# Performance work log

Measured on AMD Instinct MI355X. Metric: run time of the kernel, lower is better.

Reference implementation:

```python
import jax, jax.numpy as jnp
import numpy as np

N, D, O, E = 8192, 1024, 1024, 16

def setup_inputs() -> dict:
    key = jax.random.key(0)
    k1, k2, k3, k4 = jax.random.split(key, 4)
    scale = 1.0 / np.sqrt(D)
    x = jax.random.normal(k1, (N, D), dtype=jnp.float32)
    Wg = jax.random.normal(k2, (E, D), dtype=jnp.float32) * scale
    We = jax.random.normal(k3, (E, O, D), dtype=jnp.float32) * scale
    be = jax.random.normal(k4, (E, O), dtype=jnp.float32) * scale
    return {"x": x, "Wg": Wg, "We": We, "be": be}

def reference(x, Wg, We, be):
    # gate: softmax over experts
    gate_logits = jnp.einsum('nd,ed->ne', x, Wg)          # [N, E]
    gate_weights = jax.nn.softmax(gate_logits, axis=1)    # [N, E]
    # top-1 mask via >= max (ties keep all maxima, matching torch code)
    max_w = jnp.max(gate_weights, axis=1, keepdims=True)
    mask = (gate_weights >= max_w).astype(gate_weights.dtype)
    sw = gate_weights * mask                              # selected weights [N, E]
    # weighted sum of all-expert Linear outputs, fused (no [N,E,O] intermediate)
    out = jnp.einsum('nd,eod,ne->no', x, We, sw) + sw @ be  # [N, O]
    return (out, gate_weights)
```

## Files before the change

kernel.cpp:

```cpp
#include <hip/hip_runtime.h>
#include <hip/hip_bf16.h>

#define NROWS 8192
#define DIM   1024
#define OUTD  1024
#define NE    16
#define BM    128
#define BN    64
#define BK    32
#define MAXT  96
#define NKSTEP (DIM / BK)
#define NTILE  (OUTD / BN)
#define GATEBLKS 512
#define CONVBLKS 2048

typedef short s16x8 __attribute__((ext_vector_type(8)));
typedef float f32x4 __attribute__((ext_vector_type(4)));

__device__ __forceinline__ unsigned f2bf(float f) {
  __hip_bfloat16 h = __float2bfloat16(f);
  return (unsigned)__builtin_bit_cast(unsigned short, h);
}

__device__ __forceinline__ void gload_lds16(const void* g, void* l) {
  __builtin_amdgcn_global_load_lds(
      (const __attribute__((address_space(1))) void*)g,
      (__attribute__((address_space(3))) void*)l, 16, 0, 0);
}

__global__ __launch_bounds__(256) void convert_we_kernel(
    const float* __restrict__ W, ushort* __restrict__ o) {
  size_t base = ((size_t)blockIdx.x * 256 + threadIdx.x) * 8;
  #pragma unroll
  for (int i = 0; i < 4; ++i) {
    size_t idx = base + (size_t)i * ((size_t)CONVBLKS * 256 * 8);
    float4 a = *(const float4*)(W + idx);
    float4 c = *(const float4*)(W + idx + 4);
    unsigned w0 = f2bf(a.x) | (f2bf(a.y) << 16);
    unsigned w1 = f2bf(a.z) | (f2bf(a.w) << 16);
    unsigned w2 = f2bf(c.x) | (f2bf(c.y) << 16);
    unsigned w3 = f2bf(c.z) | (f2bf(c.w) << 16);
    *(uint4*)(o + idx) = make_uint4(w0, w1, w2, w3);
  }
}

__global__ __launch_bounds__(256) void gate_kernel(
    const float* __restrict__ x, const float* __restrict__ Wg,
    float* __restrict__ gate_out, int* __restrict__ eid,
    float* __restrict__ wsel, ushort* __restrict__ xb,
    int* __restrict__ hist_g)
{
  __shared__ __align__(16) float4 wg4[NE * 256];
  __shared__ int hist[NE];
  int t = threadIdx.x;
  int wid = t >> 6, lane = t & 63;
  if (t < NE) hist[t] = 0;
  const float4* wgg = (const float4*)Wg;
  #pragma unroll
  for (int i = 0; i < 16; ++i) wg4[t + i * 256] = wgg[t + i * 256];
  __syncthreads();

  int n0 = blockIdx.x * 16 + wid * 4;

  float acc[4][NE];
  #pragma unroll
  for (int r = 0; r < 4; ++r)
    #pragma unroll
    for (int e = 0; e < NE; ++e) acc[r][e] = 0.f;

  #pragma unroll
  for (int j = 0; j < 4; ++j) {
    float4 xv[4];
    #pragma unroll
    for (int r = 0; r < 4; ++r) {
      xv[r] = *(const float4*)(x + (size_t)(n0 + r) * DIM + j * 256 + 4 * lane);
      unsigned lo = f2bf(xv[r].x) | (f2bf(xv[r].y) << 16);
      unsigned hi = f2bf(xv[r].z) | (f2bf(xv[r].w) << 16);
      *(uint2*)(xb + (size_t)(n0 + r) * DIM + j * 256 + 4 * lane) = make_uint2(lo, hi);
    }
    #pragma unroll
    for (int e = 0; e < NE; ++e) {
      float4 w = wg4[e * 256 + j * 64 + lane];
      #pragma unroll
      for (int r = 0; r < 4; ++r)
        acc[r][e] += xv[r].x * w.x + xv[r].y * w.y + xv[r].z * w.z + xv[r].w * w.w;
    }
  }

  #pragma unroll
  for (int r = 0; r < 4; ++r) {
    int n = n0 + r;
    float v[NE];
    #pragma unroll
    for (int e = 0; e < NE; ++e) v[e] = acc[r][e];
    #pragma unroll
    for (int i = 0; i < 8; ++i) {
      float send = (lane & 32) ? v[i] : v[i + 8];
      float recv = __shfl_xor(send, 32, 64);
      v[i] = ((lane & 32) ? v[i + 8] : v[i]) + recv;
    }
    #pragma unroll
    for (int i = 0; i < 4; ++i) {
      float send = (lane & 16) ? v[i] : v[i + 4];
      float recv = __shfl_xor(send, 16, 64);
      v[i] = ((lane & 16) ? v[i + 4] : v[i]) + recv;
    }
    #pragma unroll
    for (int i = 0; i < 2; ++i) {
      float send = (lane & 8) ? v[i] : v[i + 2];
      float recv = __shfl_xor(send, 8, 64);
      v[i] = ((lane & 8) ? v[i + 2] : v[i]) + recv;
    }
    {
      float send = (lane & 4) ? v[0] : v[1];
      float recv = __shfl_xor(send, 4, 64);
      v[0] = ((lane & 4) ? v[1] : v[0]) + recv;
    }
    v[0] += __shfl_xor(v[0], 2, 64);
    v[0] += __shfl_xor(v[0], 1, 64);
    float lg = v[0];
    int e = ((lane >> 5) & 1) * 8 + ((lane >> 4) & 1) * 4 +
            ((lane >> 3) & 1) * 2 + ((lane >> 2) & 1);
    float m = lg;
    m = fmaxf(m, __shfl_xor(m, 4, 64));
    m = fmaxf(m, __shfl_xor(m, 8, 64));
    m = fmaxf(m, __shfl_xor(m, 16, 64));
    m = fmaxf(m, __shfl_xor(m, 32, 64));
    float p = expf(lg - m);
    float s = p;
    s += __shfl_xor(s, 4, 64);
    s += __shfl_xor(s, 8, 64);
    s += __shfl_xor(s, 16, 64);
    s += __shfl_xor(s, 32, 64);
    float inv = 1.f / s;
    if ((lane & 3) == 0) gate_out[(size_t)n * NE + e] = p * inv;
    unsigned long long msk = __ballot(lg == m);
    if (lane == 0) {
      int fl = __builtin_ctzll(msk);
      int ebest = ((fl >> 5) & 1) * 8 + ((fl >> 4) & 1) * 4 +
                  ((fl >> 3) & 1) * 2 + ((fl >> 2) & 1);
      eid[n] = ebest;
      wsel[n] = inv;
      atomicAdd(&hist[ebest], 1);
    }
  }
  __syncthreads();
  if (t < NE) hist_g[blockIdx.x * NE + t] = hist[t];
}

__global__ __launch_bounds__(256) void plan_kernel(
    const int* __restrict__ hist_g, int* __restrict__ offsets,
    int* __restrict__ cursors, int4* __restrict__ tiles)
{
  __shared__ int part[16][17];
  __shared__ int sh_total;
  int t = threadIdx.x;
  int e = t & 15, chunk = t >> 4;
  int s = 0;
  #pragma unroll
  for (int i = 0; i < 32; ++i) s += hist_g[(chunk * 32 + i) * NE + e];
  part[chunk][e] = s;
  __syncthreads();
  if (t < 64) {
    int lane = t;
    int c = 0;
    if (lane < NE) {
      #pragma unroll
      for (int ch = 0; ch < 16; ++ch) c += part[ch][lane];
    }
    int nt = (c + BM - 1) >> 7;
    int po = c, pt = nt;
    #pragma unroll
    for (int d = 1; d < 16; d <<= 1) {
      int oc = __shfl_up(po, d, 64);
      int ot = __shfl_up(pt, d, 64);
      if (lane >= d) { po += oc; pt += ot; }
    }
    int off = po - c, tbase = pt - nt;
    if (lane < NE) { offsets[lane] = off; cursors[lane] = off; }
    if (lane == NE - 1) { offsets[NE] = po; sh_total = pt; }
    if (lane < NE) {
      int ti = 0;
      for (int m = 0; m < c; m += BM, ++ti)
        tiles[tbase + ti] = make_int4(lane, off + m, (c - m < BM) ? (c - m) : BM, 0);
    }
  }
  __syncthreads();
  for (int i = sh_total + t; i < MAXT; i += 256)
    tiles[i] = make_int4(-1, 0, 0, 0);
}

__global__ __launch_bounds__(256) void scatter_kernel(
    const int* __restrict__ eid, int* __restrict__ cursors,
    int* __restrict__ rowids)
{
  __shared__ int h[NE];
  __shared__ int base[NE];
  int t = threadIdx.x;
  if (t < NE) h[t] = 0;
  __syncthreads();
  int n = blockIdx.x * 256 + t;
  int e = eid[n];
  int local = atomicAdd(&h[e], 1);
  __syncthreads();
  if (t < NE) base[t] = h[t] ? atomicAdd(&cursors[t], h[t]) : 0;
  __syncthreads();
  rowids[base[e] + local] = n;
}

__global__ __launch_bounds__(256, 4) void moe_gemm_kernel(
    const ushort* __restrict__ xb, const ushort* __restrict__ Web,
    const float* __restrict__ be, const int* __restrict__ rowids,
    const float* __restrict__ wsel, const int4* __restrict__ tiles,
    float* __restrict__ out)
{
  __shared__ __align__(16) char lds[3 * 12288];
  __shared__ int   rows_s[BM];
  __shared__ float w_s[BM];

  int4 ti = tiles[blockIdx.x];
  int e = ti.x;
  if (e < 0) return;
  int srow = ti.y, nvalid = ti.z;
  int t = threadIdx.x, lane = t & 63;
  int wid = t >> 6, wm = wid >> 1, wn = wid & 1;
  int ncol0 = blockIdx.y * BN;

  if (t < BM) {
    int valid = t < nvalid;
    int rid = valid ? rowids[srow + t] : 0;
    rows_s[t] = valid ? rid : -1;
    w_s[t] = valid ? wsel[rid] : 0.f;
  }

  int r1 = t >> 2, sl = t & 3;
  int r2 = r1 + 64;
  int cg = sl ^ ((r1 >> 1) & 3);
  int rida1 = (r1 < nvalid) ? rowids[srow + r1] : 0;
  int rida2 = (r2 < nvalid) ? rowids[srow + r2] : 0;
  const ushort* ap1 = xb + (size_t)rida1 * DIM + cg * 8;
  const ushort* ap2 = xb + (size_t)rida2 * DIM + cg * 8;
  const ushort* bp1 = Web + (size_t)e * OUTD * DIM + (size_t)(ncol0 + r1) * DIM + cg * 8;

  f32x4 zero = {0.f, 0.f, 0.f, 0.f};
  f32x4 acc[4][2];
  #pragma unroll
  for (int i = 0; i < 4; ++i)
    #pragma unroll
    for (int j = 0; j < 2; ++j) acc[i][j] = zero;

  auto stage = [&](int bufoff, int koff) {
    char* A = lds + bufoff;
    char* B = A + 8192;
    gload_lds16(ap1 + koff, A + t * 16);
    gload_lds16(ap2 + koff, A + 4096 + t * 16);
    gload_lds16(bp1 + koff, B + t * 16);
  };

  unsigned rl15 = lane & 15, rcg = lane >> 4;
  auto body = [&](int bufoff) {
    const char* A = lds + bufoff;
    const char* B = A + 8192;
    s16x8 af[4], bf_[2];
    #pragma unroll
    for (int f = 0; f < 4; ++f) {
      unsigned rA = wm * 64 + f * 16 + rl15;
      af[f] = *(const s16x8*)(A + rA * 64 + ((rcg ^ ((rA >> 1) & 3)) * 16));
    }
    #pragma unroll
    for (int f = 0; f < 2; ++f) {
      unsigned rB = wn * 32 + f * 16 + rl15;
      bf_[f] = *(const s16x8*)(B + rB * 64 + ((rcg ^ ((rB >> 1) & 3)) * 16));
    }
    #pragma unroll
    for (int fm = 0; fm < 4; ++fm)
      #pragma unroll
      for (int fn = 0; fn < 2; ++fn)
        acc[fm][fn] = __builtin_amdgcn_mfma_f32_16x16x32_bf16(af[fm], bf_[fn], acc[fm][fn], 0, 0, 0);
  };

  asm volatile("s_waitcnt vmcnt(0)" ::: "memory");
  stage(0, 0);
  stage(12288, BK);
  int stg = 24576, cur = 0;

  for (int ks = 0; ks < NKSTEP - 1; ++ks) {
    asm volatile("s_waitcnt vmcnt(3)" ::: "memory");
    __builtin_amdgcn_s_barrier();
    asm volatile("" ::: "memory");
    if (ks < NKSTEP - 2) {
      stage(stg, (ks + 2) * BK);
      stg = (stg == 24576) ? 0 : stg + 12288;
    }
    body(cur);
    cur = (cur == 24576) ? 0 : cur + 12288;
  }
  asm volatile("s_waitcnt vmcnt(0)" ::: "memory");
  __builtin_amdgcn_s_barrier();
  asm volatile("" ::: "memory");
  body(cur);

  int rgrp = lane >> 4;
  #pragma unroll
  for (int fn = 0; fn < 2; ++fn) {
    int col = ncol0 + wn * 32 + fn * 16 + (lane & 15);
    float bev = be[e * OUTD + col];
    #pragma unroll
    for (int fm = 0; fm < 4; ++fm) {
      #pragma unroll
      for (int j = 0; j < 4; ++j) {
        int rl = wm * 64 + fm * 16 + rgrp * 4 + j;
        int orow = rows_s[rl];
        if (orow >= 0) {
          float w = w_s[rl];
          out[(size_t)orow * OUTD + col] = w * (acc[fm][fn][j] + bev);
        }
      }
    }
  }
}

extern "C" void kernel_launch(void* const* d_in, const int* in_sizes, int n_in,
                              void* d_out, int out_size, void* d_ws, size_t ws_size,
                              hipStream_t stream) {
  const float* x  = (const float*)d_in[0];
  const float* Wg = (const float*)d_in[1];
  const float* We = (const float*)d_in[2];
  const float* be = (const float*)d_in[3];
  float* out = (float*)d_out;
  float* gate_out = out + (size_t)NROWS * OUTD;

  char* ws = (char*)d_ws;
  int*  cursors = (int*)ws;
  int*  offsets = (int*)(ws + 64);
  int4* tiles   = (int4*)(ws + 256);
  int*  hist_g  = (int*)(ws + 4096);
  int*  eidp    = (int*)(ws + 40960);
  float* wselp  = (float*)(ws + 40960 + 4 * NROWS);
  int*  rowids  = (int*)(ws + 40960 + 8 * NROWS);
  ushort* xb    = (ushort*)(ws + (1u << 20));
  ushort* Web   = (ushort*)(ws + (1u << 20) + 16777216u);

  hipLaunchKernelGGL(convert_we_kernel, dim3(CONVBLKS), dim3(256), 0, stream, We, Web);
  hipLaunchKernelGGL(gate_kernel, dim3(GATEBLKS), dim3(256), 0, stream,
                     x, Wg, gate_out, eidp, wselp, xb, hist_g);
  hipLaunchKernelGGL(plan_kernel, dim3(1), dim3(256), 0, stream,
                     hist_g, offsets, cursors, tiles);
  hipLaunchKernelGGL(scatter_kernel, dim3(NROWS / 256), dim3(256), 0, stream,
                     eidp, cursors, rowids);
  hipLaunchKernelGGL(moe_gemm_kernel, dim3(MAXT, NTILE), dim3(256), 0, stream,
                     xb, Web, be, rowids, wselp, tiles, out);
}
```

Measured before the change: 231.5 us.

## Widen MoE GEMM tile to 128x128 with 32x32 MFMA and double buffering

The grouped GEMM tile grows from 128x64 to 128x128, and the inner product switches from 16x16x32 to 32x32x16 bf16 MFMA with larger per-wave accumulators. The goal is more arithmetic intensity per LDS load and fewer global reloads of the gathered x rows across column tiles. The triple-buffered, manual-waitcnt pipeline becomes a simpler double buffer with __syncthreads, and the grid is flattened so blocks sharing a row tile run next to each other. The trade-off is higher register pressure, half as many blocks, and less overlap between loads and compute.

```diff
diff --git a/kernel.cpp b/kernel.cpp
--- a/kernel.cpp
+++ b/kernel.cpp
@@ -6,16 +6,16 @@
 #define OUTD  1024
 #define NE    16
 #define BM    128
-#define BN    64
+#define BN    128
 #define BK    32
 #define MAXT  96
 #define NKSTEP (DIM / BK)
-#define NTILE  (OUTD / BN)
+#define NCOL   (OUTD / BN)
 #define GATEBLKS 512
 #define CONVBLKS 2048
 
 typedef short s16x8 __attribute__((ext_vector_type(8)));
-typedef float f32x4 __attribute__((ext_vector_type(4)));
+typedef float f32x16 __attribute__((ext_vector_type(16)));
 
 __device__ __forceinline__ unsigned f2bf(float f) {
   __hip_bfloat16 h = __float2bfloat16(f);
@@ -214,17 +214,18 @@
     const float* __restrict__ wsel, const int4* __restrict__ tiles,
     float* __restrict__ out)
 {
-  __shared__ __align__(16) char lds[3 * 12288];
+  __shared__ __align__(16) char lds[2 * 16384];
   __shared__ int   rows_s[BM];
   __shared__ float w_s[BM];
 
-  int4 ti = tiles[blockIdx.x];
+  int rt = blockIdx.x >> 3, c = blockIdx.x & 7;
+  int4 ti = tiles[rt];
   int e = ti.x;
   if (e < 0) return;
   int srow = ti.y, nvalid = ti.z;
   int t = threadIdx.x, lane = t & 63;
   int wid = t >> 6, wm = wid >> 1, wn = wid & 1;
-  int ncol0 = blockIdx.y * BN;
+  int ncol0 = c * BN;
 
   if (t < BM) {
     int valid = t < nvalid;
@@ -240,14 +241,17 @@
   int rida2 = (r2 < nvalid) ? rowids[srow + r2] : 0;
   const ushort* ap1 = xb + (size_t)rida1 * DIM + cg * 8;
   const ushort* ap2 = xb + (size_t)rida2 * DIM + cg * 8;
-  const ushort* bp1 = Web + (size_t)e * OUTD * DIM + (size_t)(ncol0 + r1) * DIM + cg * 8;
-
-  f32x4 zero = {0.f, 0.f, 0.f, 0.f};
-  f32x4 acc[4][2];
-  #pragma unroll
-  for (int i = 0; i < 4; ++i)
-    #pragma unroll
-    for (int j = 0; j < 2; ++j) acc[i][j] = zero;
+  const ushort* bb  = Web + (size_t)e * OUTD * DIM + (size_t)ncol0 * DIM + cg * 8;
+  const ushort* bp1 = bb + (size_t)r1 * DIM;
+  const ushort* bp2 = bb + (size_t)r2 * DIM;
+
+  f32x16 acc[2][2];
+  #pragma unroll
+  for (int i = 0; i < 2; ++i)
+    #pragma unroll
+    for (int j = 0; j < 2; ++j)
+      #pragma unroll
+      for (int r = 0; r < 16; ++r) acc[i][j][r] = 0.f;
 
   auto stage = [&](int bufoff, int koff) {
     char* A = lds + bufoff;
@@ -255,66 +259,55 @@
     gload_lds16(ap1 + koff, A + t * 16);
     gload_lds16(ap2 + koff, A + 4096 + t * 16);
     gload_lds16(bp1 + koff, B + t * 16);
+    gload_lds16(bp2 + koff, B + 4096 + t * 16);
   };
 
-  unsigned rl15 = lane & 15, rcg = lane >> 4;
+  unsigned l31 = lane & 31, lhi = lane >> 5;
   auto body = [&](int bufoff) {
     const char* A = lds + bufoff;
     const char* B = A + 8192;
-    s16x8 af[4], bf_[2];
-    #pragma unroll
-    for (int f = 0; f < 4; ++f) {
-      unsigned rA = wm * 64 + f * 16 + rl15;
-      af[f] = *(const s16x8*)(A + rA * 64 + ((rcg ^ ((rA >> 1) & 3)) * 16));
-    }
-    #pragma unroll
-    for (int f = 0; f < 2; ++f) {
-      unsigned rB = wn * 32 + f * 16 + rl15;
-      bf_[f] = *(const s16x8*)(B + rB * 64 + ((rcg ^ ((rB >> 1) & 3)) * 16));
-    }
-    #pragma unroll
-    for (int fm = 0; fm < 4; ++fm)
-      #pragma unroll
-      for (int fn = 0; fn < 2; ++fn)
-        acc[fm][fn] = __builtin_amdgcn_mfma_f32_16x16x32_bf16(af[fm], bf_[fn], acc[fm][fn], 0, 0, 0);
+    s16x8 af[2][2], bfr[2][2];
+    #pragma unroll
+    for (int rb = 0; rb < 2; ++rb)
+      #pragma unroll
+      for (int ku = 0; ku < 2; ++ku) {
+        unsigned rA = wm * 64 + rb * 32 + l31;
+        unsigned slA = (unsigned)(ku * 2 + lhi) ^ ((rA >> 1) & 3);
+        af[rb][ku] = *(const s16x8*)(A + rA * 64 + slA * 16);
+        unsigned rB = wn * 64 + rb * 32 + l31;
+        unsigned slB = (unsigned)(ku * 2 + lhi) ^ ((rB >> 1) & 3);
+        bfr[rb][ku] = *(const s16x8*)(B + rB * 64 + slB * 16);
+      }
+    #pragma unroll
+    for (int ku = 0; ku < 2; ++ku)
+      #pragma unroll
+      for (int rb = 0; rb < 2; ++rb)
+        #pragma unroll
+        for (int cb = 0; cb < 2; ++cb)
+          acc[rb][cb] = __builtin_amdgcn_mfma_f32_32x32x16_bf16(
+              af[rb][ku], bfr[cb][ku], acc[rb][cb], 0, 0, 0);
   };
 
-  asm volatile("s_waitcnt vmcnt(0)" ::: "memory");
   stage(0, 0);
-  stage(12288, BK);
-  int stg = 24576, cur = 0;
-
-  for (int ks = 0; ks < NKSTEP - 1; ++ks) {
-    asm volatile("s_waitcnt vmcnt(3)" ::: "memory");
-    __builtin_amdgcn_s_barrier();
-    asm volatile("" ::: "memory");
-    if (ks < NKSTEP - 2) {
-      stage(stg, (ks + 2) * BK);
-      stg = (stg == 24576) ? 0 : stg + 12288;
-    }
-    body(cur);
-    cur = (cur == 24576) ? 0 : cur + 12288;
-  }
-  asm volatile("s_waitcnt vmcnt(0)" ::: "memory");
-  __builtin_amdgcn_s_barrier();
-  asm volatile("" ::: "memory");
-  body(cur);
-
-  int rgrp = lane >> 4;
-  #pragma unroll
-  for (int fn = 0; fn < 2; ++fn) {
-    int col = ncol0 + wn * 32 + fn * 16 + (lane & 15);
+  for (int ks = 0; ks < NKSTEP; ++ks) {
+    __syncthreads();
+    if (ks + 1 < NKSTEP) stage(((ks + 1) & 1) * 16384, (ks + 1) * BK);
+    body((ks & 1) * 16384);
+  }
+
+  #pragma unroll
+  for (int cb = 0; cb < 2; ++cb) {
+    int col = ncol0 + wn * 64 + cb * 32 + l31;
     float bev = be[e * OUTD + col];
     #pragma unroll
-    for (int fm = 0; fm < 4; ++fm) {
-      #pragma unroll
-      for (int j = 0; j < 4; ++j) {
-        int rl = wm * 64 + fm * 16 + rgrp * 4 + j;
+    for (int rb = 0; rb < 2; ++rb) {
+      #pragma unroll
+      for (int r = 0; r < 16; ++r) {
+        int rowin = (r & 3) + 8 * (r >> 2) + 4 * lhi;
+        int rl = wm * 64 + rb * 32 + rowin;
         int orow = rows_s[rl];
-        if (orow >= 0) {
-          float w = w_s[rl];
-          out[(size_t)orow * OUTD + col] = w * (acc[fm][fn][j] + bev);
-        }
+        if (orow >= 0)
+          out[(size_t)orow * OUTD + col] = w_s[rl] * (acc[rb][cb][r] + bev);
       }
     }
   }
@@ -348,6 +341,6 @@
                      hist_g, offsets, cursors, tiles);
   hipLaunchKernelGGL(scatter_kernel, dim3(NROWS / 256), dim3(256), 0, stream,
                      eidp, cursors, rowids);
-  hipLaunchKernelGGL(moe_gemm_kernel, dim3(MAXT, NTILE), dim3(256), 0, stream,
+  hipLaunchKernelGGL(moe_gemm_kernel, dim3(MAXT * 8), dim3(256), 0, stream,
                      xb, Web, be, rowids, wselp, tiles, out);
 }
```

After: 212.4 us. 1.09x faster.
